# Kernel tuning notes

Measured on AMD Instinct MI355X. Metric: run time of the kernel, lower is better.

Reference implementation:

```python
import jax, jax.numpy as jnp
import numpy as np

K = 5          # number of neighbors (self excluded)
EPS = 1e-7     # distance epsilon
Q = 0.98       # quantile for radius normalization


def _cdist(A):
    # Euclidean pairwise distances [N, N] via the matmul expansion.
    sq = jnp.sum(A * A, axis=-1)
    d2 = sq[:, None] + sq[None, :] - 2.0 * (A @ A.T)
    return jnp.sqrt(jnp.maximum(d2, 0.0))


def _lid(values):
    # values: [N, K] ascending neighbor distances; LID via log-distance ratios.
    norm = values[:, -1:]
    return -jnp.sum(jnp.log10(values) - jnp.log10(norm), axis=1)


def setup_inputs() -> dict:
    key = jax.random.key(0)
    k1, k2 = jax.random.split(key)
    X = jax.random.normal(k1, (8192, 256), dtype=jnp.float32)
    Z = jax.random.normal(k2, (8192, 64), dtype=jnp.float32)
    return {"X": X, "Z": Z}


def reference(X, Z):
    n = X.shape[0]
    normA1 = jnp.quantile(jnp.linalg.norm(X - jnp.mean(X, axis=0), axis=1), Q)
    normA2 = jnp.quantile(jnp.linalg.norm(Z - jnp.mean(Z, axis=0), axis=1), Q)

    # k-NN in X space (drop self at column 0)
    x_dist = (_cdist(X) + EPS) / normA1
    neg_vals, idx = jax.lax.top_k(-x_dist, K + 1)   # smallest K+1, ascending
    values = (-neg_vals)[:, 1:]
    nn_mask = idx[:, 1:]
    lid_X = _lid(values)

    # gather the SAME neighbor indices in Z space
    z_dist = (_cdist(Z) + EPS) / normA2
    extracted = jnp.take_along_axis(z_dist, nn_mask, axis=1)
    lid_Z = _lid(extracted)

    return jnp.sum(jnp.square(lid_X - lid_Z)) / (n * K * 10)
```

## Files before the change

### kernel.cpp

```cpp
#include <hip/hip_runtime.h>
#include <math.h>
#include <stdint.h>

#define EPS     1e-7f
#define NR      8192
#define DX      256
#define DZ      64
#define KNN     5
#define KEEP    6
#define NSPLIT  8
#define NPOOL   (NSPLIT * KEEP)
#define NCAND   16
#define JS      (NR / NSPLIT)
#define JT      64
#define NCHUNK  (JS / JT)
#define RBLK    64
#define SC1     0x7F7F7F7F
#define BIASF   256.0f

typedef float f32x4 __attribute__((ext_vector_type(4)));
typedef int   i32x8 __attribute__((ext_vector_type(8)));

__device__ __forceinline__ uint32_t umin_(uint32_t a, uint32_t b) {
    return __builtin_elementwise_min(a, b);
}
__device__ __forceinline__ uint32_t umax_(uint32_t a, uint32_t b) {
    return __builtin_elementwise_max(a, b);
}

__device__ __forceinline__ uint32_t to_e4m3(float f) {
    const uint32_t u = __float_as_uint(f);
    const uint32_t s = (u >> 24) & 0x80u;
    const int e = (int)((u >> 23) & 0xFFu) - 127;
    if (e < -10) return s;
    if (e > 8)   return s | 0x7Eu;
    const uint32_t mant = (u & 0x7FFFFFu) | 0x800000u;
    const int shift = (e < -6) ? (14 - e) : 20;
    uint32_t q = (mant + (1u << (shift - 1))) >> shift;
    int E = (e < -6) ? 0 : (e + 7);
    if (q >= 16) { q >>= 1; E += 1; }
    if (E == 0) return s | q;
    return s | ((uint32_t)E << 3) | (q & 7u);
}

__global__ __launch_bounds__(256) void split_k(const float* __restrict__ X,
                                               uint8_t* __restrict__ Xq,
                                               float* __restrict__ sqX,
                                               float* __restrict__ out) {
    if (blockIdx.x == 0 && threadIdx.x == 0) out[0] = 0.0f;
    const int row  = blockIdx.x * 4 + (threadIdx.x >> 6);
    const int lane = threadIdx.x & 63;
    const float4 v = *(const float4*)&X[(size_t)row * DX + lane * 4];
    float s = v.x * v.x + v.y * v.y + v.z * v.z + v.w * v.w;
    const uint32_t b = to_e4m3(v.x) | (to_e4m3(v.y) << 8) |
                       (to_e4m3(v.z) << 16) | (to_e4m3(v.w) << 24);
    ((uint32_t*)Xq)[(size_t)row * (DX / 4) + lane] = b;
    #pragma unroll
    for (int o = 32; o > 0; o >>= 1) s += __shfl_down(s, o);
    if (lane == 0) sqX[row] = s;
}

#define FOLD_BODY(KILL)                                                                   \
    _Pragma("unroll")                                                                     \
    for (int g = 0; g < 2; ++g) {                                                         \
        _Pragma("unroll")                                                                 \
        for (int r = 0; r < 4; ++r) {                                                     \
            const int q = g * 4 + r;                                                      \
            uint32_t c0 = (__float_as_uint(acc[0][g][r]) & 0xFFFFE000u) | (uint32_t)j0;   \
            uint32_t c1 = (__float_as_uint(acc[1][g][r]) & 0xFFFFE000u) | (uint32_t)j1;   \
            if (KILL) {                                                                   \
                const int irow = rowbase + g * 16 + quad * 4 + r;                         \
                c0 = (j0 == irow) ? 0xFFFFFFFFu : c0;                                     \
                c1 = (j1 == irow) ? 0xFFFFFFFFu : c1;                                     \
            }                                                                             \
            const uint32_t lo = umin_(c0, c1);                                            \
            const uint32_t hi = umax_(c0, c1);                                            \
            const uint32_t b0 = best[q][0], b1 = best[q][1], b2 = best[q][2],             \
                           b3 = best[q][3];                                               \
            best[q][0] = umin_(b0, lo);                                                   \
            best[q][1] = umin_(umin_(b1, hi), umax_(b0, lo));                             \
            best[q][2] = umin_(umin_(b2, umax_(b1, lo)), umax_(b0, hi));                  \
            best[q][3] = umin_(umin_(b3, umax_(b2, lo)), umax_(b1, hi));                  \
        }                                                                                 \
    }

__global__ __launch_bounds__(256, 2) void mfma_topk_k(const uint8_t* __restrict__ Xq,
                                                      const float* __restrict__ sqX,
                                                      uint32_t* __restrict__ partials) {
    __shared__ __align__(16) uint8_t smem[16384];
    __shared__ uint32_t mb2[RBLK][2][KNN];
    __shared__ __align__(16) float sq_s[JS];
    const uint4* Bv = (const uint4*)smem;

    const int tid  = threadIdx.x;
    const int w    = tid >> 6;
    const int lane = tid & 63;
    const int n    = lane & 15;
    const int quad = lane >> 4;
    const int x7   = n & 7;
    const int h    = w >> 1;
    const int sp   = w & 1;
    const int s    = blockIdx.x & 7;
    const int ib   = (blockIdx.x >> 3) * RBLK;
    const int jb0  = s * JS;
    const int rowbase = ib + h * 32;

    ((f32x4*)sq_s)[tid] = ((const f32x4*)(sqX + jb0))[tid];

    const int rel   = rowbase - jb0;
    const int cdiag = __builtin_amdgcn_readfirstlane((rel >= 0 && rel < JS) ? (rel >> 6) : -1);

    i32x8 Aq[2][2];
    #pragma unroll
    for (int g = 0; g < 2; ++g)
        #pragma unroll
        for (int kf = 0; kf < 2; ++kf)
            Aq[g][kf] = *(const i32x8*)(Xq + (size_t)(rowbase + g * 16 + n) * DX
                                        + kf * 128 + quad * 32);

    uint32_t best[8][4];
    #pragma unroll
    for (int q = 0; q < 8; ++q)
        #pragma unroll
        for (int k = 0; k < 4; ++k) best[q][k] = 0xFFFFFFFFu;

    const uint8_t* srcp[4];
    uint8_t*       dstp[4];
    #pragma unroll
    for (int u = 0; u < 4; ++u) {
        const int q  = w * 256 + u * 64 + lane;
        const int sj = q >> 4;
        const int c  = (q & 15) ^ (sj & 7);
        srcp[u] = Xq + (size_t)jb0 * DX + sj * DX + c * 16;
        dstp[u] = smem + (size_t)(w * 256 + u * 64) * 16;
    }
    int bidx[2][2][2];
    #pragma unroll
    for (int kf = 0; kf < 2; ++kf)
        #pragma unroll
        for (int si = 0; si < 2; ++si) {
            const int sj = (sp * 2 + si) * 16 + n;
            const int cb = kf * 8 + quad * 2;
            bidx[kf][si][0] = sj * 16 + (cb ^ x7);
            bidx[kf][si][1] = sj * 16 + ((cb + 1) ^ x7);
        }
    const float* sqp = sq_s + sp * 32 + n;
    int j0 = jb0 + sp * 32 + n;

    for (int jc = 0; jc < NCHUNK; ++jc) {
        __syncthreads();
        #pragma unroll
        for (int u = 0; u < 4; ++u) {
            __builtin_amdgcn_global_load_lds((const __attribute__((address_space(1))) uint32_t*)srcp[u],
                                             (__attribute__((address_space(3))) uint32_t*)dstp[u],
                                             16, 0, 0);
            srcp[u] += JT * DX;
        }
        __syncthreads();

        const float ini0 = fmaf(-0.5f, sqp[jc * JT],      -BIASF);
        const float ini1 = fmaf(-0.5f, sqp[jc * JT + 16], -BIASF);

        f32x4 acc[2][2];
        #pragma unroll
        for (int g = 0; g < 2; ++g)
            #pragma unroll
            for (int r = 0; r < 4; ++r) { acc[0][g][r] = ini0; acc[1][g][r] = ini1; }

        #pragma unroll
        for (int kf = 0; kf < 2; ++kf) {
            #pragma unroll
            for (int si = 0; si < 2; ++si) {
                union { uint4 p[2]; i32x8 v; } bb;
                bb.p[0] = Bv[bidx[kf][si][0]];
                bb.p[1] = Bv[bidx[kf][si][1]];
                acc[si][0] = __builtin_amdgcn_mfma_scale_f32_16x16x128_f8f6f4(
                                 Aq[0][kf], bb.v, acc[si][0], 0, 0, 0, SC1, 0, SC1);
                acc[si][1] = __builtin_amdgcn_mfma_scale_f32_16x16x128_f8f6f4(
                                 Aq[1][kf], bb.v, acc[si][1], 0, 0, 0, SC1, 0, SC1);
            }
        }

        const int j1 = j0 + 16;
        if (jc != cdiag) {
            FOLD_BODY(0)
        } else {
            FOLD_BODY(1)
        }
        j0 += JT;
    }

    #pragma unroll
    for (int q = 0; q < 8; ++q) {
        const uint32_t s0 = best[q][0], s1 = best[q][1], s2 = best[q][2], s3 = best[q][3];
        const uint32_t t0 = __shfl_xor(s0, 1);
        const uint32_t t1 = __shfl_xor(s1, 1);
        const uint32_t t2 = __shfl_xor(s2, 1);
        const uint32_t t3 = __shfl_xor(s3, 1);
        uint32_t a0 = umin_(s0, t0);
        uint32_t a1 = umin_(umin_(s1, t1), umax_(s0, t0));
        uint32_t a2 = umin_(umin_(s2, t2), umin_(umax_(s1, t0), umax_(s0, t1)));
        uint32_t a3 = umin_(umin_(s3, t3),
                            umin_(umax_(s2, t0), umin_(umax_(s1, t1), umax_(s0, t2))));
        uint32_t a4 = umin_(umin_(umax_(s3, t0), umax_(s2, t1)),
                            umin_(umax_(s1, t2), umax_(s0, t3)));
        #pragma unroll
        for (int mask = 2; mask <= 8; mask <<= 1) {
            const uint32_t b0 = __shfl_xor(a0, mask);
            const uint32_t b1 = __shfl_xor(a1, mask);
            const uint32_t b2 = __shfl_xor(a2, mask);
            const uint32_t b3 = __shfl_xor(a3, mask);
            const uint32_t b4 = __shfl_xor(a4, mask);
            const uint32_t c0 = umin_(a0, b0);
            const uint32_t c1 = umin_(umin_(a1, b1), umax_(a0, b0));
            const uint32_t c2 = umin_(umin_(a2, b2), umin_(umax_(a0, b1), umax_(a1, b0)));
            const uint32_t c3 = umin_(umin_(a3, b3),
                                      umin_(umax_(a1, b1), umin_(umax_(a0, b2), umax_(a2, b0))));
            const uint32_t c4 = umin_(umin_(a4, b4),
                                      umin_(umin_(umax_(a0, b3), umax_(a1, b2)),
                                            umin_(umax_(a2, b1), umax_(a3, b0))));
            a0 = c0; a1 = c1; a2 = c2; a3 = c3; a4 = c4;
        }
        const int rloc = h * 32 + (q >> 2) * 16 + quad * 4 + (q & 3);
        uint32_t v = a0;
        v = (n == 1) ? a1 : v;
        v = (n == 2) ? a2 : v;
        v = (n == 3) ? a3 : v;
        v = (n == 4) ? a4 : v;
        if (n < KNN) mb2[rloc][sp][n] = v;
    }
    __syncthreads();

    if (tid < RBLK) {
        const uint32_t a0 = mb2[tid][0][0], a1 = mb2[tid][0][1], a2 = mb2[tid][0][2],
                       a3 = mb2[tid][0][3], a4 = mb2[tid][0][4];
        const uint32_t b0 = mb2[tid][1][0], b1 = mb2[tid][1][1], b2 = mb2[tid][1][2],
                       b3 = mb2[tid][1][3], b4 = mb2[tid][1][4];
        uint32_t o[KEEP];
        o[0] = umin_(a0, b0);
        o[1] = umin_(umin_(a1, b1), umax_(a0, b0));
        o[2] = umin_(umin_(a2, b2), umin_(umax_(a0, b1), umax_(a1, b0)));
        o[3] = umin_(umin_(a3, b3), umin_(umax_(a1, b1), umin_(umax_(a0, b2), umax_(a2, b0))));
        o[4] = umin_(umin_(a4, b4), umin_(umin_(umax_(a0, b3), umax_(a1, b2)),
                                          umin_(umax_(a2, b1), umax_(a3, b0))));
        o[5] = umin_(umin_(umax_(a0, b4), umax_(a4, b0)),
                     umin_(umax_(a1, b3), umin_(umax_(a2, b2), umax_(a3, b1))));
        #pragma unroll
        for (int k = 0; k < KEEP; ++k)
            partials[(size_t)(ib + tid) * NPOOL + s * KEEP + k] = o[k];
    }
}

__global__ __launch_bounds__(256) void finalize_k(const uint32_t* __restrict__ parts,
                                                  const float* __restrict__ X,
                                                  const float* __restrict__ Z,
                                                  const float* __restrict__ sqX,
                                                  float* __restrict__ out) {
    __shared__ float wsum[4];
    const int wv   = threadIdx.x >> 6;
    const int lane = threadIdx.x & 63;
    const int i    = blockIdx.x * 4 + wv;

    uint32_t v = (lane < NPOOL) ? parts[(size_t)i * NPOOL + lane] : 0xFFFFFFFFu;
    #pragma unroll
    for (int kk = 2; kk <= 64; kk <<= 1) {
        #pragma unroll
        for (int jj = kk >> 1; jj > 0; jj >>= 1) {
            const uint32_t o = __shfl_xor(v, jj);
            const bool keepmin = ((lane & kk) == 0) == ((lane & jj) == 0);
            v = keepmin ? umin_(v, o) : umax_(v, o);
        }
    }

    const float4 xi = *(const float4*)(X + (size_t)i * DX + lane * 4);

    float p[16];
    #pragma unroll
    for (int c = 0; c < NCAND; ++c) {
        const int jc = (int)(__shfl(v, c) & 0x1FFFu);
        const float4 xj = *(const float4*)(X + (size_t)jc * DX + lane * 4);
        p[c] = fmaf(xi.x, xj.x, fmaf(xi.y, xj.y, fmaf(xi.z, xj.z, xi.w * xj.w)));
    }
    #pragma unroll
    for (int c = 0; c < NCAND; ++c) {
        p[c] += __shfl_xor(p[c], 1);
        p[c] += __shfl_xor(p[c], 2);
        p[c] += __shfl_xor(p[c], 4);
        p[c] += __shfl_xor(p[c], 8);
    }
    const int cs = lane & 15;
    float dotv = p[0];
    dotv = (cs == 1)  ? p[1]  : dotv;
    dotv = (cs == 2)  ? p[2]  : dotv;
    dotv = (cs == 3)  ? p[3]  : dotv;
    dotv = (cs == 4)  ? p[4]  : dotv;
    dotv = (cs == 5)  ? p[5]  : dotv;
    dotv = (cs == 6)  ? p[6]  : dotv;
    dotv = (cs == 7)  ? p[7]  : dotv;
    dotv = (cs == 8)  ? p[8]  : dotv;
    dotv = (cs == 9)  ? p[9]  : dotv;
    dotv = (cs == 10) ? p[10] : dotv;
    dotv = (cs == 11) ? p[11] : dotv;
    dotv = (cs == 12) ? p[12] : dotv;
    dotv = (cs == 13) ? p[13] : dotv;
    dotv = (cs == 14) ? p[14] : dotv;
    dotv = (cs == 15) ? p[15] : dotv;
    dotv += __shfl_xor(dotv, 16);
    dotv += __shfl_xor(dotv, 32);

    unsigned long long k16 = 0xFFFFFFFFFFFFFFFFull;
    const int jl = (int)(v & 0x1FFFu);
    if (lane < NCAND) {
        const float d2x = (sqX[i] + sqX[jl]) - 2.0f * dotv;
        k16 = ((unsigned long long)__float_as_uint(d2x) << 32) | (unsigned)jl;
    }
    #pragma unroll
    for (int kk = 2; kk <= 16; kk <<= 1) {
        #pragma unroll
        for (int jj = kk >> 1; jj > 0; jj >>= 1) {
            const unsigned long long o = __shfl_xor(k16, jj);
            const bool keepmin = ((lane & kk) == 0) == ((lane & jj) == 0);
            k16 = keepmin ? (k16 < o ? k16 : o) : (k16 < o ? o : k16);
        }
    }

    const float d2k = __uint_as_float((uint32_t)(k16 >> 32));
    const int   jk  = (int)(k16 & 0x1FFFull);
    float lkx = 0.0f;
    if (lane < KNN) lkx = log10f(sqrtf(fmaxf(d2k, 0.0f)) + EPS);
    const float l4x = __shfl(lkx, KNN - 1);
    float sx = lkx;
    sx += __shfl_xor(sx, 1);
    sx += __shfl_xor(sx, 2);
    sx += __shfl_xor(sx, 4);

    const float zi = Z[(size_t)i * DZ + lane];
    float zsum = 0.0f, l4z = 0.0f;
    #pragma unroll
    for (int k = 0; k < KNN; ++k) {
        const int jz = __shfl(jk, k);
        const float zj = Z[(size_t)jz * DZ + lane];
        const float d = zi - zj;
        float s = d * d;
        s += __shfl_xor(s, 1);
        s += __shfl_xor(s, 2);
        s += __shfl_xor(s, 4);
        s += __shfl_xor(s, 8);
        s += __shfl_xor(s, 16);
        s += __shfl_xor(s, 32);
        const float lk = log10f(sqrtf(fmaxf(s, 0.0f)) + EPS);
        zsum += lk;
        if (k == KNN - 1) l4z = lk;
    }

    if (lane == 0) {
        const float lx = -(__shfl(sx, 0) - (float)KNN * l4x);
        const float lz = -(zsum - (float)KNN * l4z);
        const float diff = lx - lz;
        wsum[wv] = diff * diff * (1.0f / ((float)NR * KNN * 10.0f));
    }
    __syncthreads();
    if (threadIdx.x == 0)
        atomicAdd(out, wsum[0] + wsum[1] + wsum[2] + wsum[3]);
}

extern "C" void kernel_launch(void* const* d_in, const int* in_sizes, int n_in,
                              void* d_out, int out_size, void* d_ws, size_t ws_size,
                              hipStream_t stream) {
    const float* X = (const float*)d_in[0];
    const float* Z = (const float*)d_in[1];
    float* out = (float*)d_out;

    char* ws = (char*)d_ws;
    float*     sqX      = (float*)ws;
    uint32_t*  partials = (uint32_t*)(ws + 32768);
    uint8_t*   Xq       = (uint8_t*)(ws + 32768 + 2097152);

    split_k<<<NR / 4, 256, 0, stream>>>(X, Xq, sqX, out);
    mfma_topk_k<<<(NR / RBLK) * NSPLIT, 256, 0, stream>>>(Xq, sqX, partials);
    finalize_k<<<NR / 4, 256, 0, stream>>>(partials, X, Z, sqX, out);
}
```

Before: 138.4 us.

## Load B tiles directly from global into registers, splitting columns across waves

Removes the shared-memory staging of the column tile (global_load_lds plus two block barriers per chunk). Each wave pair now owns a disjoint half of the column split and loads its fp8 B fragments and squared norms straight from global memory into registers. Because the two sp waves now see different columns, the per-wave merge keeps six candidates instead of five so the cross-wave merge stays exact. This trades synchronisation and LDS traffic for uncached, less coalesced global loads, with no sharing of B data across the two row halves except through L1/L2.

```diff
diff --git a/kernel.cpp b/kernel.cpp
--- a/kernel.cpp
+++ b/kernel.cpp
@@ -12,14 +12,14 @@
 #define NPOOL   (NSPLIT * KEEP)
 #define NCAND   16
 #define JS      (NR / NSPLIT)
-#define JT      64
-#define NCHUNK  (JS / JT)
+#define JT      32
+#define NCHUNK  (JS / 2 / JT)
 #define RBLK    64
 #define SC1     0x7F7F7F7F
 #define BIASF   256.0f
 
-typedef float f32x4 __attribute__((ext_vector_type(4)));
-typedef int   i32x8 __attribute__((ext_vector_type(8)));
+typedef float  f32x4 __attribute__((ext_vector_type(4)));
+typedef int    i32x8 __attribute__((ext_vector_type(8)));
 
 __device__ __forceinline__ uint32_t umin_(uint32_t a, uint32_t b) {
     return __builtin_elementwise_min(a, b);
@@ -87,28 +87,23 @@
 __global__ __launch_bounds__(256, 2) void mfma_topk_k(const uint8_t* __restrict__ Xq,
                                                       const float* __restrict__ sqX,
                                                       uint32_t* __restrict__ partials) {
-    __shared__ __align__(16) uint8_t smem[16384];
-    __shared__ uint32_t mb2[RBLK][2][KNN];
-    __shared__ __align__(16) float sq_s[JS];
-    const uint4* Bv = (const uint4*)smem;
+    __shared__ uint32_t mb2[RBLK][2][KEEP];
 
     const int tid  = threadIdx.x;
     const int w    = tid >> 6;
     const int lane = tid & 63;
     const int n    = lane & 15;
     const int quad = lane >> 4;
-    const int x7   = n & 7;
     const int h    = w >> 1;
     const int sp   = w & 1;
     const int s    = blockIdx.x & 7;
     const int ib   = (blockIdx.x >> 3) * RBLK;
-    const int jb0  = s * JS;
+    const int jb0  = s * JS + sp * (JS / 2);
     const int rowbase = ib + h * 32;
 
-    ((f32x4*)sq_s)[tid] = ((const f32x4*)(sqX + jb0))[tid];
-
     const int rel   = rowbase - jb0;
-    const int cdiag = __builtin_amdgcn_readfirstlane((rel >= 0 && rel < JS) ? (rel >> 6) : -1);
+    const int cdiag = __builtin_amdgcn_readfirstlane(
+                          (rel >= 0 && rel < JS / 2) ? (rel >> 5) : -1);
 
     i32x8 Aq[2][2];
     #pragma unroll
@@ -124,62 +119,52 @@
         #pragma unroll
         for (int k = 0; k < 4; ++k) best[q][k] = 0xFFFFFFFFu;
 
-    const uint8_t* srcp[4];
-    uint8_t*       dstp[4];
-    #pragma unroll
-    for (int u = 0; u < 4; ++u) {
-        const int q  = w * 256 + u * 64 + lane;
-        const int sj = q >> 4;
-        const int c  = (q & 15) ^ (sj & 7);
-        srcp[u] = Xq + (size_t)jb0 * DX + sj * DX + c * 16;
-        dstp[u] = smem + (size_t)(w * 256 + u * 64) * 16;
-    }
-    int bidx[2][2][2];
-    #pragma unroll
-    for (int kf = 0; kf < 2; ++kf)
-        #pragma unroll
-        for (int si = 0; si < 2; ++si) {
-            const int sj = (sp * 2 + si) * 16 + n;
-            const int cb = kf * 8 + quad * 2;
-            bidx[kf][si][0] = sj * 16 + (cb ^ x7);
-            bidx[kf][si][1] = sj * 16 + ((cb + 1) ^ x7);
-        }
-    const float* sqp = sq_s + sp * 32 + n;
-    int j0 = jb0 + sp * 32 + n;
+    const uint8_t* bp0 = Xq + (size_t)(jb0 + n) * DX + quad * 32;
+    const uint8_t* bp1 = bp0 + 16 * DX;
+    const float*   sqp = sqX + jb0 + n;
+    int j0 = jb0 + n;
 
     for (int jc = 0; jc < NCHUNK; ++jc) {
-        __syncthreads();
-        #pragma unroll
-        for (int u = 0; u < 4; ++u) {
-            __builtin_amdgcn_global_load_lds((const __attribute__((address_space(1))) uint32_t*)srcp[u],
-                                             (__attribute__((address_space(3))) uint32_t*)dstp[u],
-                                             16, 0, 0);
-            srcp[u] += JT * DX;
-        }
-        __syncthreads();
-
-        const float ini0 = fmaf(-0.5f, sqp[jc * JT],      -BIASF);
-        const float ini1 = fmaf(-0.5f, sqp[jc * JT + 16], -BIASF);
+        const uint4 b00 = *(const uint4*)(bp0);
+        const uint4 b01 = *(const uint4*)(bp0 + 16);
+        const uint4 b02 = *(const uint4*)(bp0 + 128);
+        const uint4 b03 = *(const uint4*)(bp0 + 144);
+        const uint4 b10 = *(const uint4*)(bp1);
+        const uint4 b11 = *(const uint4*)(bp1 + 16);
+        const uint4 b12 = *(const uint4*)(bp1 + 128);
+        const uint4 b13 = *(const uint4*)(bp1 + 144);
+
+        const float ini0 = fmaf(-0.5f, sqp[0],  -BIASF);
+        const float ini1 = fmaf(-0.5f, sqp[16], -BIASF);
 
         f32x4 acc[2][2];
         #pragma unroll
-        for (int g = 0; g < 2; ++g)
-            #pragma unroll
-            for (int r = 0; r < 4; ++r) { acc[0][g][r] = ini0; acc[1][g][r] = ini1; }
-
-        #pragma unroll
-        for (int kf = 0; kf < 2; ++kf) {
-            #pragma unroll
-            for (int si = 0; si < 2; ++si) {
-                union { uint4 p[2]; i32x8 v; } bb;
-                bb.p[0] = Bv[bidx[kf][si][0]];
-                bb.p[1] = Bv[bidx[kf][si][1]];
-                acc[si][0] = __builtin_amdgcn_mfma_scale_f32_16x16x128_f8f6f4(
-                                 Aq[0][kf], bb.v, acc[si][0], 0, 0, 0, SC1, 0, SC1);
-                acc[si][1] = __builtin_amdgcn_mfma_scale_f32_16x16x128_f8f6f4(
-                                 Aq[1][kf], bb.v, acc[si][1], 0, 0, 0, SC1, 0, SC1);
-            }
-        }
+        for (int r = 0; r < 4; ++r) {
+            acc[0][0][r] = ini0; acc[0][1][r] = ini0;
+            acc[1][0][r] = ini1; acc[1][1][r] = ini1;
+        }
+
+        union U { uint4 p[2]; i32x8 v; } u;
+        u.p[0] = b00; u.p[1] = b01;
+        acc[0][0] = __builtin_amdgcn_mfma_scale_f32_16x16x128_f8f6f4(
+                        Aq[0][0], u.v, acc[0][0], 0, 0, 0, SC1, 0, SC1);
+        acc[0][1] = __builtin_amdgcn_mfma_scale_f32_16x16x128_f8f6f4(
+                        Aq[1][0], u.v, acc[0][1], 0, 0, 0, SC1, 0, SC1);
+        u.p[0] = b02; u.p[1] = b03;
+        acc[0][0] = __builtin_amdgcn_mfma_scale_f32_16x16x128_f8f6f4(
+                        Aq[0][1], u.v, acc[0][0], 0, 0, 0, SC1, 0, SC1);
+        acc[0][1] = __builtin_amdgcn_mfma_scale_f32_16x16x128_f8f6f4(
+                        Aq[1][1], u.v, acc[0][1], 0, 0, 0, SC1, 0, SC1);
+        u.p[0] = b10; u.p[1] = b11;
+        acc[1][0] = __builtin_amdgcn_mfma_scale_f32_16x16x128_f8f6f4(
+                        Aq[0][0], u.v, acc[1][0], 0, 0, 0, SC1, 0, SC1);
+        acc[1][1] = __builtin_amdgcn_mfma_scale_f32_16x16x128_f8f6f4(
+                        Aq[1][0], u.v, acc[1][1], 0, 0, 0, SC1, 0, SC1);
+        u.p[0] = b12; u.p[1] = b13;
+        acc[1][0] = __builtin_amdgcn_mfma_scale_f32_16x16x128_f8f6f4(
+                        Aq[0][1], u.v, acc[1][0], 0, 0, 0, SC1, 0, SC1);
+        acc[1][1] = __builtin_amdgcn_mfma_scale_f32_16x16x128_f8f6f4(
+                        Aq[1][1], u.v, acc[1][1], 0, 0, 0, SC1, 0, SC1);
 
         const int j1 = j0 + 16;
         if (jc != cdiag) {
@@ -187,7 +172,7 @@
         } else {
             FOLD_BODY(1)
         }
-        j0 += JT;
+        bp0 += JT * DX; bp1 += JT * DX; sqp += JT; j0 += JT;
     }
 
     #pragma unroll
@@ -204,6 +189,7 @@
                             umin_(umax_(s2, t0), umin_(umax_(s1, t1), umax_(s0, t2))));
         uint32_t a4 = umin_(umin_(umax_(s3, t0), umax_(s2, t1)),
                             umin_(umax_(s1, t2), umax_(s0, t3)));
+        uint32_t a5 = umin_(umax_(s3, t1), umin_(umax_(s2, t2), umax_(s1, t3)));
         #pragma unroll
         for (int mask = 2; mask <= 8; mask <<= 1) {
             const uint32_t b0 = __shfl_xor(a0, mask);
@@ -211,15 +197,20 @@
             const uint32_t b2 = __shfl_xor(a2, mask);
             const uint32_t b3 = __shfl_xor(a3, mask);
             const uint32_t b4 = __shfl_xor(a4, mask);
+            const uint32_t b5 = __shfl_xor(a5, mask);
             const uint32_t c0 = umin_(a0, b0);
             const uint32_t c1 = umin_(umin_(a1, b1), umax_(a0, b0));
-            const uint32_t c2 = umin_(umin_(a2, b2), umin_(umax_(a0, b1), umax_(a1, b0)));
+            const uint32_t c2 = umin_(umin_(a2, b2), umin_(umax_(a1, b0), umax_(a0, b1)));
             const uint32_t c3 = umin_(umin_(a3, b3),
-                                      umin_(umax_(a1, b1), umin_(umax_(a0, b2), umax_(a2, b0))));
+                                      umin_(umax_(a2, b0), umin_(umax_(a1, b1), umax_(a0, b2))));
             const uint32_t c4 = umin_(umin_(a4, b4),
-                                      umin_(umin_(umax_(a0, b3), umax_(a1, b2)),
-                                            umin_(umax_(a2, b1), umax_(a3, b0))));
-            a0 = c0; a1 = c1; a2 = c2; a3 = c3; a4 = c4;
+                                      umin_(umin_(umax_(a3, b0), umax_(a2, b1)),
+                                            umin_(umax_(a1, b2), umax_(a0, b3))));
+            const uint32_t c5 = umin_(umin_(a5, b5),
+                                      umin_(umin_(umax_(a4, b0), umax_(a3, b1)),
+                                            umin_(umax_(a2, b2),
+                                                  umin_(umax_(a1, b3), umax_(a0, b4)))));
+            a0 = c0; a1 = c1; a2 = c2; a3 = c3; a4 = c4; a5 = c5;
         }
         const int rloc = h * 32 + (q >> 2) * 16 + quad * 4 + (q & 3);
         uint32_t v = a0;
@@ -227,24 +218,26 @@
         v = (n == 2) ? a2 : v;
         v = (n == 3) ? a3 : v;
         v = (n == 4) ? a4 : v;
-        if (n < KNN) mb2[rloc][sp][n] = v;
+        v = (n == 5) ? a5 : v;
+        if (n < KEEP) mb2[rloc][sp][n] = v;
     }
     __syncthreads();
 
     if (tid < RBLK) {
         const uint32_t a0 = mb2[tid][0][0], a1 = mb2[tid][0][1], a2 = mb2[tid][0][2],
-                       a3 = mb2[tid][0][3], a4 = mb2[tid][0][4];
+                       a3 = mb2[tid][0][3], a4 = mb2[tid][0][4], a5 = mb2[tid][0][5];
         const uint32_t b0 = mb2[tid][1][0], b1 = mb2[tid][1][1], b2 = mb2[tid][1][2],
-                       b3 = mb2[tid][1][3], b4 = mb2[tid][1][4];
+                       b3 = mb2[tid][1][3], b4 = mb2[tid][1][4], b5 = mb2[tid][1][5];
         uint32_t o[KEEP];
         o[0] = umin_(a0, b0);
         o[1] = umin_(umin_(a1, b1), umax_(a0, b0));
-        o[2] = umin_(umin_(a2, b2), umin_(umax_(a0, b1), umax_(a1, b0)));
-        o[3] = umin_(umin_(a3, b3), umin_(umax_(a1, b1), umin_(umax_(a0, b2), umax_(a2, b0))));
-        o[4] = umin_(umin_(a4, b4), umin_(umin_(umax_(a0, b3), umax_(a1, b2)),
-                                          umin_(umax_(a2, b1), umax_(a3, b0))));
-        o[5] = umin_(umin_(umax_(a0, b4), umax_(a4, b0)),
-                     umin_(umax_(a1, b3), umin_(umax_(a2, b2), umax_(a3, b1))));
+        o[2] = umin_(umin_(a2, b2), umin_(umax_(a1, b0), umax_(a0, b1)));
+        o[3] = umin_(umin_(a3, b3), umin_(umax_(a2, b0), umin_(umax_(a1, b1), umax_(a0, b2))));
+        o[4] = umin_(umin_(a4, b4), umin_(umin_(umax_(a3, b0), umax_(a2, b1)),
+                                          umin_(umax_(a1, b2), umax_(a0, b3))));
+        o[5] = umin_(umin_(a5, b5), umin_(umin_(umax_(a4, b0), umax_(a3, b1)),
+                                          umin_(umax_(a2, b2),
+                                                umin_(umax_(a1, b3), umax_(a0, b4)))));
         #pragma unroll
         for (int k = 0; k < KEEP; ++k)
             partials[(size_t)(ib + tid) * NPOOL + s * KEEP + k] = o[k];
```

Result: slower. 171.1 us (+23.7%).
